# Performance work log

Measured on AMD Instinct MI355X. Metric: run time of the kernel, lower is better.

Reference implementation:

```python
import jax, jax.numpy as jnp
import numpy as np

EPS = 1e-5
SLOPE = 0.01  # LeakyReLU default
C = 512
C2 = C // 2
B, D, W, H = 2, 16, 16, 16


def _leaky(x):
    return jnp.where(x >= 0, x, SLOPE * x)


def _bn_c(x, g, b, rm, rv):
    # per-channel BN (eval mode) over axis 1 of a (B,C,...) tensor
    shape = (1, -1) + (1,) * (x.ndim - 2)
    inv = jax.lax.rsqrt(rv + EPS)
    return (x - rm.reshape(shape)) * (inv * g).reshape(shape) + b.reshape(shape)


def _bn_s(x, g, b, rm, rv):
    # scalar-feature BatchNorm1d(1) in eval mode
    return (x - rm[0]) * (jax.lax.rsqrt(rv[0] + EPS) * g[0]) + b[0]


def setup_inputs() -> dict:
    key = jax.random.key(0)
    ks = jax.random.split(key, 8)
    s = 0.02
    inp = {
        'x': jax.random.normal(ks[0], (B, C, D, W, H), jnp.float32),
        'topo_prompt': jax.random.normal(ks[1], (D, W, H, 6), jnp.float32) * s,
        # edge_aggregation_func: Linear(6,1)+BN1d(1)
        'w_ea': jax.random.normal(ks[2], (1, 6), jnp.float32) * s,
        'b_ea': jnp.zeros((1,), jnp.float32),
        'g_ea': jnp.ones((1,), jnp.float32), 'be_ea': jnp.zeros((1,), jnp.float32),
        'rm_ea': jnp.zeros((1,), jnp.float32), 'rv_ea': jnp.ones((1,), jnp.float32),
        # vertex_update_func: Linear(2C, C/2)+BN1d(C/2)
        'w_v': jax.random.normal(ks[3], (C2, 2 * C), jnp.float32) * s,
        'b_v': jnp.zeros((C2,), jnp.float32),
        'g_v': jnp.ones((C2,), jnp.float32), 'be_v': jnp.zeros((C2,), jnp.float32),
        'rm_v': jnp.zeros((C2,), jnp.float32), 'rv_v': jnp.ones((C2,), jnp.float32),
        # edge_update_func: Linear(2C, C/2)+BN1d(C/2)
        'w_e': jax.random.normal(ks[4], (C2, 2 * C), jnp.float32) * s,
        'b_e': jnp.zeros((C2,), jnp.float32),
        'g_e': jnp.ones((C2,), jnp.float32), 'be_e': jnp.zeros((C2,), jnp.float32),
        'rm_e': jnp.zeros((C2,), jnp.float32), 'rv_e': jnp.ones((C2,), jnp.float32),
        # update_edge_reduce_func: Linear(6,1)+BN1d(1)
        'w_r': jax.random.normal(ks[5], (1, 6), jnp.float32) * s,
        'b_r': jnp.zeros((1,), jnp.float32),
        'g_r': jnp.ones((1,), jnp.float32), 'be_r': jnp.zeros((1,), jnp.float32),
        'rm_r': jnp.zeros((1,), jnp.float32), 'rv_r': jnp.ones((1,), jnp.float32),
        # final_aggregation_layer: Conv3d(3C/2 -> C, k=1, bias=False)+BN3d(C)
        'w_f': jax.random.normal(ks[6], (C, C + C2), jnp.float32) * s,
        'g_f': jnp.ones((C,), jnp.float32), 'be_f': jnp.zeros((C,), jnp.float32),
        'rm_f': jnp.zeros((C,), jnp.float32), 'rv_f': jnp.ones((C,), jnp.float32),
    }
    return inp


def reference(x, topo_prompt,
              w_ea, b_ea, g_ea, be_ea, rm_ea, rv_ea,
              w_v, b_v, g_v, be_v, rm_v, rv_v,
              w_e, b_e, g_e, be_e, rm_e, rv_e,
              w_r, b_r, g_r, be_r, rm_r, rv_r,
              w_f, g_f, be_f, rm_f, rv_f):
    # 6-neighbor circular shifts: cat((x[-1:], x[:-1])) == roll(+1); cat((x[1:], x[:1])) == roll(-1)
    shifts = jnp.stack([
        jnp.roll(x, 1, axis=2), jnp.roll(x, -1, axis=2),
        jnp.roll(x, 1, axis=3), jnp.roll(x, -1, axis=3),
        jnp.roll(x, 1, axis=4), jnp.roll(x, -1, axis=4),
    ], axis=-1)  # (B,C,D,W,H,6)
    edge = shifts * x[..., None] + topo_prompt  # topo_prompt (D,W,H,6) broadcasts

    # edge aggregation: Linear(6->1) + BN1d(1) + LeakyReLU
    agg = jnp.einsum('bcdwhk,k->bcdwh', edge, w_ea[0]) + b_ea[0]
    agg = _leaky(_bn_s(agg, g_ea, be_ea, rm_ea, rv_ea))  # (B,C,D,W,H)

    # vertex update: Linear(2C->C/2) + BN + LeakyReLU
    feat_v = jnp.concatenate([x, agg], axis=1)  # (B,2C,D,W,H)
    uv = jnp.einsum('bcdwh,oc->bodwh', feat_v, w_v) + b_v[None, :, None, None, None]
    uv = _leaky(_bn_c(uv, g_v, be_v, rm_v, rv_v))  # (B,C/2,D,W,H)

    # edge update: cat(vertex x6, edge) on channel dim -> Linear(2C->C/2) + BN + LeakyReLU
    vrep = jnp.broadcast_to(x[..., None], x.shape + (6,))
    feat_e = jnp.concatenate([vrep, edge], axis=1)  # (B,2C,D,W,H,6)
    ue = jnp.einsum('bcdwhk,oc->bodwhk', feat_e, w_e) + b_e[None, :, None, None, None, None]
    ue = _leaky(_bn_c(ue, g_e, be_e, rm_e, rv_e))  # (B,C/2,D,W,H,6)

    # reduce 6 neighbors: Linear(6->1) + BN1d(1) + LeakyReLU
    ur = jnp.einsum('bodwhk,k->bodwh', ue, w_r[0]) + b_r[0]
    ur = _leaky(_bn_s(ur, g_r, be_r, rm_r, rv_r))  # (B,C/2,D,W,H)

    update_feature = uv * ur

    # final 1x1x1 conv (bias=False) + BN3d + LeakyReLU
    fused = jnp.concatenate([x, update_feature], axis=1)  # (B,3C/2,D,W,H)
    out = jnp.einsum('bcdwh,oc->bodwh', fused, w_f)
    out = _leaky(_bn_c(out, g_f, be_f, rm_f, rv_f))
    return out
```

## Files before the change

### kernel.cpp

```cpp
#include <hip/hip_runtime.h>

#define BATCH 2
#define C 512
#define C2 256
#define V 4096
#define NROWS 8192
#define EPS 1e-5f
#define SLOPE 0.01f
#define LDSW 40

typedef __bf16 bf16;
typedef __bf16 bf16x8 __attribute__((ext_vector_type(8)));
typedef __bf16 bf16x4 __attribute__((ext_vector_type(4)));
typedef float  f32x4  __attribute__((ext_vector_type(4)));

__device__ __forceinline__ float leaky(float x) { return x >= 0.f ? x : SLOPE * x; }

__device__ __forceinline__ int nbr(int v, int k) {
    int h = v & 15, w = (v >> 4) & 15, d = v >> 8;
    switch (k) {
        case 0: return (v & 0x0FF) | (((d + 15) & 15) << 8);
        case 1: return (v & 0x0FF) | (((d + 1) & 15) << 8);
        case 2: return (v & 0xF0F) | (((w + 15) & 15) << 4);
        case 3: return (v & 0xF0F) | (((w + 1) & 15) << 4);
        case 4: return (v & 0xFF0) | ((h + 15) & 15);
        default: return (v & 0xFF0) | ((h + 1) & 15);
    }
}

__device__ __forceinline__ void st_lds(bf16* lds, uint4 v, int t) {
    *(uint4*)(lds + (t >> 2) * LDSW + (t & 3) * 8) = v;
}

__device__ __forceinline__ void mm32(const bf16* A, const bf16* B,
                                     f32x4 (&acc)[4][2], int abase, int bbase,
                                     int lr, int kg)
{
    bf16x8 af[4], bv[2];
    #pragma unroll
    for (int mb = 0; mb < 4; mb++)
        af[mb] = *(const bf16x8*)(A + (abase + mb * 16 + lr) * LDSW + kg * 8);
    #pragma unroll
    for (int nb = 0; nb < 2; nb++)
        bv[nb] = *(const bf16x8*)(B + (bbase + nb * 16 + lr) * LDSW + kg * 8);
    #pragma unroll
    for (int mb = 0; mb < 4; mb++)
        #pragma unroll
        for (int nb = 0; nb < 2; nb++)
            acc[mb][nb] = __builtin_amdgcn_mfma_f32_16x16x32_bf16(af[mb], bv[nb], acc[mb][nb], 0, 0, 0);
}

__global__ __launch_bounds__(256) void k_prep(
    const float* wv, const float* we, const float* wf,
    const float* w_ea, const float* b_ea, const float* g_ea, const float* be_ea,
    const float* rm_ea, const float* rv_ea,
    const float* b_v, const float* g_v, const float* be_v, const float* rm_v, const float* rv_v,
    const float* b_e, const float* g_e, const float* be_e, const float* rm_e, const float* rv_e,
    const float* w_r, const float* b_r, const float* g_r, const float* be_r,
    const float* rm_r, const float* rv_r,
    const float* g_f, const float* be_f, const float* rm_f, const float* rv_f,
    float* P, float* obv, float* obe, float* obf,
    bf16* wmain, bf16* we2, bf16* owf)
{
    int i = blockIdx.x * 256 + threadIdx.x;
    if (i < 524288) {
        int o = i >> 10, c = i & 1023;
        float val;
        if (o < 256) val = rsqrtf(rv_v[o] + EPS) * g_v[o] * wv[(size_t)o * 1024 + c];
        else {
            int oe = o - 256;
            val = (c < 512) ? rsqrtf(rv_e[oe] + EPS) * g_e[oe] * we[(size_t)oe * 1024 + c] : 0.f;
        }
        wmain[i] = (bf16)val;
    } else if (i < 655360) {
        int j = i - 524288; int o = j >> 9, c = j & 511;
        we2[j] = (bf16)(rsqrtf(rv_e[o] + EPS) * g_e[o] * we[(size_t)o * 1024 + 512 + c]);
    } else if (i < 1048576) {
        int j = i - 655360; int o = j / 768;
        owf[j] = (bf16)(rsqrtf(rv_f[o] + EPS) * g_f[o] * wf[j]);
    }
    if (blockIdx.x == 0) {
        int t = threadIdx.x;
        obf[t]       = be_f[t]       - rsqrtf(rv_f[t]       + EPS) * g_f[t]       * rm_f[t];
        obf[t + 256] = be_f[t + 256] - rsqrtf(rv_f[t + 256] + EPS) * g_f[t + 256] * rm_f[t + 256];
        float sv = rsqrtf(rv_v[t] + EPS) * g_v[t];
        obv[t] = sv * (b_v[t] - rm_v[t]) + be_v[t];
        float se = rsqrtf(rv_e[t] + EPS) * g_e[t];
        obe[t] = se * (b_e[t] - rm_e[t]) + be_e[t];
        if (t < 6) {
            float sa = rsqrtf(rv_ea[0] + EPS) * g_ea[0];
            P[t] = sa * w_ea[t];
            float sr = rsqrtf(rv_r[0] + EPS) * g_r[0];
            P[8 + t] = sr * w_r[t];
        }
        if (t == 6) {
            float sa = rsqrtf(rv_ea[0] + EPS) * g_ea[0];
            P[6] = sa * (b_ea[0] - rm_ea[0]) + be_ea[0];
            float sr = rsqrtf(rv_r[0] + EPS) * g_r[0];
            P[14] = sr * (b_r[0] - rm_r[0]) + be_r[0];
        }
    }
}

__global__ __launch_bounds__(256) void k_aggT(
    const float* __restrict__ x, const float* __restrict__ topo,
    const float* __restrict__ P,
    bf16* __restrict__ xT, bf16* __restrict__ aggT)
{
    __shared__ float T[64][65];
    const int t = threadIdx.x;
    const int b = blockIdx.z, ct = blockIdx.y * 64, vt = blockIdx.x * 64;
    const int cl = t >> 2;
    const int c  = ct + cl;
    const int vl0 = (t & 3) * 16;
    const int v0 = vt + vl0;
    const int w = (v0 >> 4) & 15, d = v0 >> 8;
    const float* xp = x + (((size_t)b * C + c) << 12);

    float xr[16], xd0[16], xd1[16], xw0[16], xw1[16];
    #pragma unroll
    for (int i = 0; i < 4; i++) {
        float4 a;
        a = ((const float4*)(xp + v0))[i];                        xr [4*i]=a.x; xr [4*i+1]=a.y; xr [4*i+2]=a.z; xr [4*i+3]=a.w;
        a = ((const float4*)(xp + (((d+15)&15)<<8) + (w<<4)))[i]; xd0[4*i]=a.x; xd0[4*i+1]=a.y; xd0[4*i+2]=a.z; xd0[4*i+3]=a.w;
        a = ((const float4*)(xp + (((d+ 1)&15)<<8) + (w<<4)))[i]; xd1[4*i]=a.x; xd1[4*i+1]=a.y; xd1[4*i+2]=a.z; xd1[4*i+3]=a.w;
        a = ((const float4*)(xp + (d<<8) + (((w+15)&15)<<4)))[i]; xw0[4*i]=a.x; xw0[4*i+1]=a.y; xw0[4*i+2]=a.z; xw0[4*i+3]=a.w;
        a = ((const float4*)(xp + (d<<8) + (((w+ 1)&15)<<4)))[i]; xw1[4*i]=a.x; xw1[4*i+1]=a.y; xw1[4*i+2]=a.z; xw1[4*i+3]=a.w;
    }

    #pragma unroll
    for (int p = 0; p < 2; ++p) {
        float val[16];
        if (p == 0) {
            #pragma unroll
            for (int j = 0; j < 16; j++) val[j] = xr[j];
        } else {
            #pragma unroll
            for (int j = 0; j < 16; j++) {
                const float* tp = topo + (size_t)(v0 + j) * 6;
                float s = P[6];
                s = fmaf(P[0], fmaf(xd0[j], xr[j], tp[0]), s);
                s = fmaf(P[1], fmaf(xd1[j], xr[j], tp[1]), s);
                s = fmaf(P[2], fmaf(xw0[j], xr[j], tp[2]), s);
                s = fmaf(P[3], fmaf(xw1[j], xr[j], tp[3]), s);
                s = fmaf(P[4], fmaf(xr[(j+15)&15], xr[j], tp[4]), s);
                s = fmaf(P[5], fmaf(xr[(j+ 1)&15], xr[j], tp[5]), s);
                val[j] = leaky(s);
            }
        }
        __syncthreads();
        #pragma unroll
        for (int j = 0; j < 16; j++) T[cl][vl0 + j] = val[j];
        __syncthreads();
        const int vr = t >> 2, c0 = (t & 3) * 16;
        bf16x8 lo, hi;
        #pragma unroll
        for (int i = 0; i < 8; i++) {
            lo[i] = (bf16)T[c0 + i][vr];
            hi[i] = (bf16)T[c0 + 8 + i][vr];
        }
        bf16* dst = (p == 0) ? xT : aggT;
        bf16* dp = dst + ((size_t)(b << 12) + vt + vr) * C + ct + c0;
        *(bf16x8*)dp = lo;
        *(bf16x8*)(dp + 8) = hi;
    }
}

__global__ __launch_bounds__(512, 4) void k_main(
    const bf16* __restrict__ xT, const bf16* __restrict__ aggT,
    const bf16* __restrict__ wm, const float* __restrict__ bvp,
    bf16* __restrict__ uvT, float* __restrict__ sxe)
{
    __shared__ __align__(16) bf16 L[2][2][128 * LDSW];
    const int t = threadIdx.x, lane = t & 63, wid = t >> 6;
    const int wmi = wid >> 2, wni = wid & 3;
    const int lr = lane & 15, kg = lane >> 4;
    const int n0 = blockIdx.x * 128, m0 = blockIdx.y * 128;
    const int srow = t >> 2, scol = (t & 3) * 8;

    f32x4 acc[4][2];
    #pragma unroll
    for (int mb = 0; mb < 4; mb++)
        #pragma unroll
        for (int nb = 0; nb < 2; nb++) acc[mb][nb] = 0.f;

    uint4 sA, sB;
    auto issue = [&](int s) {
        sA = *(const uint4*)(wm + (size_t)(m0 + srow) * 1024 + s * 32 + scol);
        const bf16* bs = (s < 16) ? xT : aggT;
        sB = *(const uint4*)(bs + (size_t)(n0 + srow) * C + (s & 15) * 32 + scol);
    };

    issue(0);
    st_lds(L[0][0], sA, t); st_lds(L[0][1], sB, t);
    issue(1);
    __syncthreads();
    #pragma unroll 1
    for (int s = 0; s < 32; ++s) {
        mm32(L[s & 1][0], L[s & 1][1], acc, wmi * 64, wni * 32, lr, kg);
        if (s + 1 < 32) {
            st_lds(L[(s + 1) & 1][0], sA, t); st_lds(L[(s + 1) & 1][1], sB, t);
            if (s + 2 < 32) issue(s + 2);
            __syncthreads();
        }
    }

    if (m0 < 256) {
        f32x4 bvv[4];
        #pragma unroll
        for (int mb = 0; mb < 4; mb++)
            bvv[mb] = *(const f32x4*)(bvp + m0 + wmi * 64 + mb * 16 + kg * 4);
        #pragma unroll
        for (int mb = 0; mb < 4; mb++)
            #pragma unroll
            for (int nb = 0; nb < 2; nb++) {
                const int col = n0 + wni * 32 + nb * 16 + lr;
                const int o = m0 + wmi * 64 + mb * 16 + kg * 4;
                bf16x4 o4;
                #pragma unroll
                for (int q = 0; q < 4; q++)
                    o4[q] = (bf16)leaky(acc[mb][nb][q] + bvv[mb][q]);
                *(bf16x4*)(uvT + (size_t)col * C2 + o) = o4;
            }
    } else {
        #pragma unroll
        for (int mb = 0; mb < 4; mb++)
            #pragma unroll
            for (int nb = 0; nb < 2; nb++) {
                const int col = n0 + wni * 32 + nb * 16 + lr;
                const int o = (m0 - 256) + wmi * 64 + mb * 16 + kg * 4;
                *(f32x4*)(sxe + (size_t)col * C2 + o) = acc[mb][nb];
            }
    }
}

__global__ __launch_bounds__(512, 4) void k_edge(
    const bf16* __restrict__ xT, const bf16* __restrict__ we2,
    const float* __restrict__ topo, bf16* __restrict__ se)
{
    __shared__ __align__(16) bf16 L[2][2][128 * LDSW];
    const int t = threadIdx.x, lane = t & 63, wid = t >> 6;
    const int wmi = wid >> 2, wni = wid & 3;
    const int lr = lane & 15, kg = lane >> 4;
    const int n0 = blockIdx.x * 128, m0 = blockIdx.y * 128;
    const int kk = n0 >> 13;
    const int srow = t >> 2, scol = (t & 3) * 8;
    const int r = (n0 & 8191) + srow;
    const int bb = r >> 12, vv = r & 4095;
    const int rn = (bb << 12) | nbr(vv, kk);
    const float tp = topo[vv * 6 + kk];

    f32x4 acc[4][2];
    #pragma unroll
    for (int mb = 0; mb < 4; mb++)
        #pragma unroll
        for (int nb = 0; nb < 2; nb++) acc[mb][nb] = 0.f;

    uint4 sA, sB, sBn;
    auto issue = [&](int s) {
        sA  = *(const uint4*)(we2 + (size_t)(m0 + srow) * 512 + s * 32 + scol);
        sB  = *(const uint4*)(xT + (size_t)r  * C + s * 32 + scol);
        sBn = *(const uint4*)(xT + (size_t)rn * C + s * 32 + scol);
    };
    auto commitB = [&](bf16* lds) {
        bf16x8 xa = *(const bf16x8*)&sB;
        bf16x8 xn = *(const bf16x8*)&sBn;
        bf16x8 e;
        #pragma unroll
        for (int i = 0; i < 8; i++)
            e[i] = (bf16)fmaf((float)xa[i], (float)xn[i], tp);
        *(bf16x8*)(lds + (t >> 2) * LDSW + (t & 3) * 8) = e;
    };

    issue(0);
    st_lds(L[0][0], sA, t); commitB(L[0][1]);
    issue(1);
    __syncthreads();
    #pragma unroll 1
    for (int s = 0; s < 16; ++s) {
        mm32(L[s & 1][0], L[s & 1][1], acc, wmi * 64, wni * 32, lr, kg);
        if (s + 1 < 16) {
            st_lds(L[(s + 1) & 1][0], sA, t); commitB(L[(s + 1) & 1][1]);
            if (s + 2 < 16) issue(s + 2);
            __syncthreads();
        }
    }

    #pragma unroll
    for (int mb = 0; mb < 4; mb++)
        #pragma unroll
        for (int nb = 0; nb < 2; nb++) {
            const int col = n0 + wni * 32 + nb * 16 + lr;
            const int rout = col & 8191;
            const int o = m0 + wmi * 64 + mb * 16 + kg * 4;
            bf16x4 o4;
            #pragma unroll
            for (int q = 0; q < 4; q++) o4[q] = (bf16)acc[mb][nb][q];
            *(bf16x4*)(se + ((size_t)kk * NROWS + rout) * C2 + o) = o4;
        }
}

__global__ __launch_bounds__(256) void k_comb(
    const float* __restrict__ sxe, const bf16* __restrict__ se,
    const bf16* __restrict__ uvT, const float* __restrict__ bep,
    const float* __restrict__ P, bf16* __restrict__ updT)
{
    const int g = blockIdx.x * 256 + threadIdx.x;
    const int row = g >> 5, o0 = (g & 31) * 8;
    const size_t base = (size_t)row * C2 + o0;

    f32x4 sx0 = *(const f32x4*)(sxe + base);
    f32x4 sx1 = *(const f32x4*)(sxe + base + 4);
    f32x4 be0 = *(const f32x4*)(bep + o0);
    f32x4 be1 = *(const f32x4*)(bep + o0 + 4);
    float ur[8] = {};
    #pragma unroll
    for (int k = 0; k < 6; k++) {
        bf16x8 s8 = *(const bf16x8*)(se + (size_t)k * NROWS * C2 + base);
        const float wrk = P[8 + k];
        #pragma unroll
        for (int i = 0; i < 4; i++) {
            ur[i]     = fmaf(wrk, leaky(sx0[i] + (float)s8[i]     + be0[i]), ur[i]);
            ur[i + 4] = fmaf(wrk, leaky(sx1[i] + (float)s8[i + 4] + be1[i]), ur[i + 4]);
        }
    }
    const float brp = P[14];
    bf16x8 uv8 = *(const bf16x8*)(uvT + base);
    bf16x8 o8;
    #pragma unroll
    for (int i = 0; i < 8; i++)
        o8[i] = (bf16)((float)uv8[i] * leaky(ur[i] + brp));
    *(bf16x8*)(updT + base) = o8;
}

__global__ __launch_bounds__(512, 4) void k_out(
    const bf16* __restrict__ xT, const bf16* __restrict__ updT,
    const bf16* __restrict__ wf, const float* __restrict__ bfp,
    float* __restrict__ out)
{
    __shared__ __align__(16) bf16 L[2][2][128 * LDSW];
    const int t = threadIdx.x, lane = t & 63, wid = t >> 6;
    const int wmi = wid >> 2, wni = wid & 3;
    const int lr = lane & 15, kg = lane >> 4;
    const int n0 = blockIdx.x * 128, m0 = blockIdx.y * 128;
    const int srow = t >> 2, scol = (t & 3) * 8;

    f32x4 acc[4][2];
    #pragma unroll
    for (int mb = 0; mb < 4; mb++)
        #pragma unroll
        for (int nb = 0; nb < 2; nb++) acc[mb][nb] = 0.f;

    uint4 sA, sB;
    auto issue = [&](int s) {
        sA = *(const uint4*)(wf + (size_t)(m0 + srow) * 768 + s * 32 + scol);
        if (s < 16) sB = *(const uint4*)(xT   + (size_t)(n0 + srow) * C  + s * 32 + scol);
        else        sB = *(const uint4*)(updT + (size_t)(n0 + srow) * C2 + (s - 16) * 32 + scol);
    };

    issue(0);
    st_lds(L[0][0], sA, t); st_lds(L[0][1], sB, t);
    issue(1);
    __syncthreads();
    #pragma unroll 1
    for (int s = 0; s < 24; ++s) {
        mm32(L[s & 1][0], L[s & 1][1], acc, wmi * 64, wni * 32, lr, kg);
        if (s + 1 < 24) {
            st_lds(L[(s + 1) & 1][0], sA, t); st_lds(L[(s + 1) & 1][1], sB, t);
            if (s + 2 < 24) issue(s + 2);
            __syncthreads();
        }
    }

    f32x4 bfv[4];
    #pragma unroll
    for (int mb = 0; mb < 4; mb++)
        bfv[mb] = *(const f32x4*)(bfp + m0 + wmi * 64 + mb * 16 + kg * 4);
    #pragma unroll
    for (int mb = 0; mb < 4; mb++)
        #pragma unroll
        for (int nb = 0; nb < 2; nb++) {
            const int col = n0 + wni * 32 + nb * 16 + lr;
            const int b = col >> 12, v = col & 4095;
            const int o = m0 + wmi * 64 + mb * 16 + kg * 4;
            #pragma unroll
            for (int q = 0; q < 4; q++)
                out[(((size_t)b * C + o + q) << 12) + v] = leaky(acc[mb][nb][q] + bfv[mb][q]);
        }
}

extern "C" void kernel_launch(void* const* d_in, const int* in_sizes, int n_in,
                              void* d_out, int out_size, void* d_ws, size_t ws_size,
                              hipStream_t stream)
{
    const float* x    = (const float*)d_in[0];
    const float* topo = (const float*)d_in[1];
    const float* w_ea = (const float*)d_in[2];
    const float* b_ea = (const float*)d_in[3];
    const float* g_ea = (const float*)d_in[4];
    const float* be_ea= (const float*)d_in[5];
    const float* rm_ea= (const float*)d_in[6];
    const float* rv_ea= (const float*)d_in[7];
    const float* w_v  = (const float*)d_in[8];
    const float* b_v  = (const float*)d_in[9];
    const float* g_v  = (const float*)d_in[10];
    const float* be_v = (const float*)d_in[11];
    const float* rm_v = (const float*)d_in[12];
    const float* rv_v = (const float*)d_in[13];
    const float* w_e  = (const float*)d_in[14];
    const float* b_e  = (const float*)d_in[15];
    const float* g_e  = (const float*)d_in[16];
    const float* be_e = (const float*)d_in[17];
    const float* rm_e = (const float*)d_in[18];
    const float* rv_e = (const float*)d_in[19];
    const float* w_r  = (const float*)d_in[20];
    const float* b_r  = (const float*)d_in[21];
    const float* g_r  = (const float*)d_in[22];
    const float* be_r = (const float*)d_in[23];
    const float* rm_r = (const float*)d_in[24];
    const float* rv_r = (const float*)d_in[25];
    const float* w_f  = (const float*)d_in[26];
    const float* g_f  = (const float*)d_in[27];
    const float* be_f = (const float*)d_in[28];
    const float* rm_f = (const float*)d_in[29];
    const float* rv_f = (const float*)d_in[30];

    char* base = (char*)d_ws;
    size_t off = 0;
    auto take = [&](size_t bytes) { size_t r = off; off = (off + bytes + 255) & ~(size_t)255; return r; };
    float* P    = (float*)(base + take(64 * 4));
    float* bvp  = (float*)(base + take(256 * 4));
    float* bep  = (float*)(base + take(256 * 4));
    float* bfp  = (float*)(base + take(512 * 4));
    bf16*  wmp  = (bf16*)(base + take((size_t)524288 * 2));
    bf16*  we2p = (bf16*)(base + take((size_t)131072 * 2));
    bf16*  wfp  = (bf16*)(base + take((size_t)393216 * 2));
    bf16*  xT   = (bf16*)(base + take((size_t)NROWS * C * 2));
    bf16*  aggT = (bf16*)(base + take((size_t)NROWS * C * 2));
    bf16*  uvT  = (bf16*)(base + take((size_t)NROWS * C2 * 2));
    bf16*  updT = (bf16*)(base + take((size_t)NROWS * C2 * 2));
    float* sxe  = (float*)(base + take((size_t)NROWS * C2 * 4));
    bf16*  se   = (bf16*)(base + take((size_t)6 * NROWS * C2 * 2));

    k_prep<<<4096, 256, 0, stream>>>(
        w_v, w_e, w_f,
        w_ea, b_ea, g_ea, be_ea, rm_ea, rv_ea,
        b_v, g_v, be_v, rm_v, rv_v,
        b_e, g_e, be_e, rm_e, rv_e,
        w_r, b_r, g_r, be_r, rm_r, rv_r,
        g_f, be_f, rm_f, rv_f,
        P, bvp, bep, bfp, wmp, we2p, wfp);

    k_aggT<<<dim3(64, 8, 2), 256, 0, stream>>>(x, topo, P, xT, aggT);

    k_main<<<dim3(64, 4), 512, 0, stream>>>(xT, aggT, wmp, bvp, uvT, sxe);
    k_edge<<<dim3(384, 2), 512, 0, stream>>>(xT, we2p, topo, se);
    k_comb<<<dim3(NROWS * C2 / 8 / 256), 256, 0, stream>>>(sxe, se, uvT, bep, P, updT);
    k_out<<<dim3(64, 4), 512, 0, stream>>>(xT, updT, wfp, bfp, (float*)d_out);
}
```

Before: 101.4 us.

## Merge vertex and edge GEMMs into one launch with register-direct B operands

Replaces the separate k_main and k_edge launches with a single k_gemm1 grid. Blocks are split by index between the vertex/x-projection GEMM and the six-neighbor edge GEMM. The B operand is no longer staged in LDS: each wave loads its activation fragments straight from global memory into registers in MFMA layout, and only the weight tile goes through double-buffered LDS. It also trims the k-loop for the sxe half to 16 steps and moves to 256-thread blocks with a 4x4 MFMA tile per wave. This should cut launch overhead, LDS traffic and the tail imbalance between the two kernels, at the cost of more VGPRs and uncoalesced 16-byte global loads for B.

```diff
diff --git a/kernel.cpp b/kernel.cpp
--- a/kernel.cpp
+++ b/kernel.cpp
@@ -166,138 +166,156 @@
     }
 }
 
-__global__ __launch_bounds__(512, 4) void k_main(
+template<bool MAIN>
+__device__ __forceinline__ void gemm_body(
+    int m0, int n0, int kk, int nsteps,
+    const bf16* __restrict__ wA, int ldA,
     const bf16* __restrict__ xT, const bf16* __restrict__ aggT,
-    const bf16* __restrict__ wm, const float* __restrict__ bvp,
-    bf16* __restrict__ uvT, float* __restrict__ sxe)
-{
-    __shared__ __align__(16) bf16 L[2][2][128 * LDSW];
-    const int t = threadIdx.x, lane = t & 63, wid = t >> 6;
-    const int wmi = wid >> 2, wni = wid & 3;
+    const float* __restrict__ topo, const float* __restrict__ bvp,
+    bf16* __restrict__ uvT, float* __restrict__ sxe, bf16* __restrict__ se,
+    bf16 (*A)[128 * LDSW])
+{
+    const int t = threadIdx.x, lane = t & 63;
+    const int wv = t >> 6, wmi = wv >> 1, wni = wv & 1;
     const int lr = lane & 15, kg = lane >> 4;
-    const int n0 = blockIdx.x * 128, m0 = blockIdx.y * 128;
-    const int srow = t >> 2, scol = (t & 3) * 8;
-
-    f32x4 acc[4][2];
-    #pragma unroll
-    for (int mb = 0; mb < 4; mb++)
-        #pragma unroll
-        for (int nb = 0; nb < 2; nb++) acc[mb][nb] = 0.f;
-
-    uint4 sA, sB;
-    auto issue = [&](int s) {
-        sA = *(const uint4*)(wm + (size_t)(m0 + srow) * 1024 + s * 32 + scol);
-        const bf16* bs = (s < 16) ? xT : aggT;
-        sB = *(const uint4*)(bs + (size_t)(n0 + srow) * C + (s & 15) * 32 + scol);
-    };
-
-    issue(0);
-    st_lds(L[0][0], sA, t); st_lds(L[0][1], sB, t);
-    issue(1);
+
+    const bf16* pB[4]; const bf16* pB2[4]; float tp[4]; int colv[4];
+    #pragma unroll
+    for (int nb = 0; nb < 4; nb++) {
+        int row = n0 + wni * 64 + nb * 16 + lr;
+        colv[nb] = row;
+        pB[nb] = xT + (size_t)row * C + kg * 8;
+        if (MAIN) {
+            pB2[nb] = aggT + (size_t)row * C + kg * 8;
+        } else {
+            int v = row & 4095, bb = row >> 12;
+            pB2[nb] = xT + (size_t)((bb << 12) | nbr(v, kk)) * C + kg * 8;
+            tp[nb] = topo[v * 6 + kk];
+        }
+    }
+
+    f32x4 acc[4][4];
+    #pragma unroll
+    for (int mb = 0; mb < 4; mb++)
+        #pragma unroll
+        for (int nb = 0; nb < 4; nb++) acc[mb][nb] = 0.f;
+
+    const int arow = t >> 1, acol = (t & 1) * 16;
+    const bf16* pA = wA + (size_t)(m0 + arow) * ldA + acol;
+
+    uint4 a0 = *(const uint4*)(pA);
+    uint4 a1 = *(const uint4*)(pA + 8);
+    uint4 bA[4], bN[4];
+    #pragma unroll
+    for (int nb = 0; nb < 4; nb++) {
+        bA[nb] = *(const uint4*)(pB[nb]);
+        if (!MAIN) bN[nb] = *(const uint4*)(pB2[nb]);
+    }
+    *(uint4*)(&A[0][arow * LDSW + acol])     = a0;
+    *(uint4*)(&A[0][arow * LDSW + acol + 8]) = a1;
     __syncthreads();
+
     #pragma unroll 1
-    for (int s = 0; s < 32; ++s) {
-        mm32(L[s & 1][0], L[s & 1][1], acc, wmi * 64, wni * 32, lr, kg);
-        if (s + 1 < 32) {
-            st_lds(L[(s + 1) & 1][0], sA, t); st_lds(L[(s + 1) & 1][1], sB, t);
-            if (s + 2 < 32) issue(s + 2);
-            __syncthreads();
-        }
-    }
-
-    if (m0 < 256) {
-        f32x4 bvv[4];
+    for (int s = 0; s < nsteps; ++s) {
+        bf16x8 Bc[4];
+        #pragma unroll
+        for (int nb = 0; nb < 4; nb++) {
+            if (MAIN) {
+                Bc[nb] = *(bf16x8*)&bA[nb];
+            } else {
+                bf16x8 xa = *(bf16x8*)&bA[nb], xn = *(bf16x8*)&bN[nb];
+                #pragma unroll
+                for (int i = 0; i < 8; i++)
+                    Bc[nb][i] = (bf16)fmaf((float)xa[i], (float)xn[i], tp[nb]);
+            }
+        }
+        if (s + 1 < nsteps) {
+            const int sc = s + 1;
+            a0 = *(const uint4*)(pA + sc * 32);
+            a1 = *(const uint4*)(pA + sc * 32 + 8);
+            const int off = (sc & 15) * 32;
+            #pragma unroll
+            for (int nb = 0; nb < 4; nb++) {
+                const bf16* src = (MAIN && sc >= 16) ? pB2[nb] : pB[nb];
+                bA[nb] = *(const uint4*)(src + off);
+                if (!MAIN) bN[nb] = *(const uint4*)(pB2[nb] + off);
+            }
+        }
+        bf16x8 af[4];
         #pragma unroll
         for (int mb = 0; mb < 4; mb++)
-            bvv[mb] = *(const f32x4*)(bvp + m0 + wmi * 64 + mb * 16 + kg * 4);
+            af[mb] = *(const bf16x8*)(&A[s & 1][(wmi * 64 + mb * 16 + lr) * LDSW + kg * 8]);
         #pragma unroll
         for (int mb = 0; mb < 4; mb++)
             #pragma unroll
-            for (int nb = 0; nb < 2; nb++) {
-                const int col = n0 + wni * 32 + nb * 16 + lr;
+            for (int nb = 0; nb < 4; nb++)
+                acc[mb][nb] = __builtin_amdgcn_mfma_f32_16x16x32_bf16(af[mb], Bc[nb], acc[mb][nb], 0, 0, 0);
+        if (s + 1 < nsteps) {
+            *(uint4*)(&A[(s + 1) & 1][arow * LDSW + acol])     = a0;
+            *(uint4*)(&A[(s + 1) & 1][arow * LDSW + acol + 8]) = a1;
+        }
+        __syncthreads();
+    }
+
+    if (MAIN) {
+        if (m0 < 256) {
+            #pragma unroll
+            for (int mb = 0; mb < 4; mb++) {
                 const int o = m0 + wmi * 64 + mb * 16 + kg * 4;
+                f32x4 bv4 = *(const f32x4*)(bvp + o);
+                #pragma unroll
+                for (int nb = 0; nb < 4; nb++) {
+                    bf16x4 o4;
+                    #pragma unroll
+                    for (int q = 0; q < 4; q++)
+                        o4[q] = (bf16)leaky(acc[mb][nb][q] + bv4[q]);
+                    *(bf16x4*)(uvT + (size_t)colv[nb] * C2 + o) = o4;
+                }
+            }
+        } else {
+            #pragma unroll
+            for (int mb = 0; mb < 4; mb++) {
+                const int o = (m0 - 256) + wmi * 64 + mb * 16 + kg * 4;
+                #pragma unroll
+                for (int nb = 0; nb < 4; nb++)
+                    *(f32x4*)(sxe + (size_t)colv[nb] * C2 + o) = acc[mb][nb];
+            }
+        }
+    } else {
+        #pragma unroll
+        for (int mb = 0; mb < 4; mb++) {
+            const int o = m0 + wmi * 64 + mb * 16 + kg * 4;
+            #pragma unroll
+            for (int nb = 0; nb < 4; nb++) {
                 bf16x4 o4;
                 #pragma unroll
-                for (int q = 0; q < 4; q++)
-                    o4[q] = (bf16)leaky(acc[mb][nb][q] + bvv[mb][q]);
-                *(bf16x4*)(uvT + (size_t)col * C2 + o) = o4;
-            }
+                for (int q = 0; q < 4; q++) o4[q] = (bf16)acc[mb][nb][q];
+                *(bf16x4*)(se + ((size_t)kk * NROWS + colv[nb]) * C2 + o) = o4;
+            }
+        }
+    }
+}
+
+__global__ __launch_bounds__(256, 3) void k_gemm1(
+    const bf16* __restrict__ xT, const bf16* __restrict__ aggT,
+    const bf16* __restrict__ wm, const bf16* __restrict__ we2,
+    const float* __restrict__ bvp, const float* __restrict__ topo,
+    bf16* __restrict__ uvT, float* __restrict__ sxe, bf16* __restrict__ se)
+{
+    __shared__ __align__(16) bf16 A[2][128 * LDSW];
+    const int bid = blockIdx.x;
+    if (bid < 256) {
+        const int m0 = (bid >> 6) * 128, n0 = (bid & 63) * 128;
+        const int nsteps = (m0 < 256) ? 32 : 16;
+        gemm_body<true>(m0, n0, 0, nsteps, wm, 1024, xT, aggT, topo, bvp,
+                        uvT, sxe, nullptr, A);
     } else {
-        #pragma unroll
-        for (int mb = 0; mb < 4; mb++)
-            #pragma unroll
-            for (int nb = 0; nb < 2; nb++) {
-                const int col = n0 + wni * 32 + nb * 16 + lr;
-                const int o = (m0 - 256) + wmi * 64 + mb * 16 + kg * 4;
-                *(f32x4*)(sxe + (size_t)col * C2 + o) = acc[mb][nb];
-            }
-    }
-}
-
-__global__ __launch_bounds__(512, 4) void k_edge(
-    const bf16* __restrict__ xT, const bf16* __restrict__ we2,
-    const float* __restrict__ topo, bf16* __restrict__ se)
-{
-    __shared__ __align__(16) bf16 L[2][2][128 * LDSW];
-    const int t = threadIdx.x, lane = t & 63, wid = t >> 6;
-    const int wmi = wid >> 2, wni = wid & 3;
-    const int lr = lane & 15, kg = lane >> 4;
-    const int n0 = blockIdx.x * 128, m0 = blockIdx.y * 128;
-    const int kk = n0 >> 13;
-    const int srow = t >> 2, scol = (t & 3) * 8;
-    const int r = (n0 & 8191) + srow;
-    const int bb = r >> 12, vv = r & 4095;
-    const int rn = (bb << 12) | nbr(vv, kk);
-    const float tp = topo[vv * 6 + kk];
-
-    f32x4 acc[4][2];
-    #pragma unroll
-    for (int mb = 0; mb < 4; mb++)
-        #pragma unroll
-        for (int nb = 0; nb < 2; nb++) acc[mb][nb] = 0.f;
-
-    uint4 sA, sB, sBn;
-    auto issue = [&](int s) {
-        sA  = *(const uint4*)(we2 + (size_t)(m0 + srow) * 512 + s * 32 + scol);
-        sB  = *(const uint4*)(xT + (size_t)r  * C + s * 32 + scol);
-        sBn = *(const uint4*)(xT + (size_t)rn * C + s * 32 + scol);
-    };
-    auto commitB = [&](bf16* lds) {
-        bf16x8 xa = *(const bf16x8*)&sB;
-        bf16x8 xn = *(const bf16x8*)&sBn;
-        bf16x8 e;
-        #pragma unroll
-        for (int i = 0; i < 8; i++)
-            e[i] = (bf16)fmaf((float)xa[i], (float)xn[i], tp);
-        *(bf16x8*)(lds + (t >> 2) * LDSW + (t & 3) * 8) = e;
-    };
-
-    issue(0);
-    st_lds(L[0][0], sA, t); commitB(L[0][1]);
-    issue(1);
-    __syncthreads();
-    #pragma unroll 1
-    for (int s = 0; s < 16; ++s) {
-        mm32(L[s & 1][0], L[s & 1][1], acc, wmi * 64, wni * 32, lr, kg);
-        if (s + 1 < 16) {
-            st_lds(L[(s + 1) & 1][0], sA, t); commitB(L[(s + 1) & 1][1]);
-            if (s + 2 < 16) issue(s + 2);
-            __syncthreads();
-        }
-    }
-
-    #pragma unroll
-    for (int mb = 0; mb < 4; mb++)
-        #pragma unroll
-        for (int nb = 0; nb < 2; nb++) {
-            const int col = n0 + wni * 32 + nb * 16 + lr;
-            const int rout = col & 8191;
-            const int o = m0 + wmi * 64 + mb * 16 + kg * 4;
-            bf16x4 o4;
-            #pragma unroll
-            for (int q = 0; q < 4; q++) o4[q] = (bf16)acc[mb][nb][q];
-            *(bf16x4*)(se + ((size_t)kk * NROWS + rout) * C2 + o) = o4;
-        }
+        const int e = bid - 256;
+        const int m0 = (e / 384) * 128;
+        const int r = e % 384, kk = r >> 6, n0 = (r & 63) * 128;
+        gemm_body<false>(m0, n0, kk, 16, we2, 512, xT, aggT, topo, bvp,
+                         nullptr, nullptr, se, A);
+    }
 }
 
 __global__ __launch_bounds__(256) void k_comb(
@@ -453,8 +471,7 @@
 
     k_aggT<<<dim3(64, 8, 2), 256, 0, stream>>>(x, topo, P, xT, aggT);
 
-    k_main<<<dim3(64, 4), 512, 0, stream>>>(xT, aggT, wmp, bvp, uvT, sxe);
-    k_edge<<<dim3(384, 2), 512, 0, stream>>>(xT, we2p, topo, se);
+    k_gemm1<<<dim3(1024), 256, 0, stream>>>(xT, aggT, wmp, we2p, bvp, topo, uvT, sxe, se);
     k_comb<<<dim3(NROWS * C2 / 8 / 256), 256, 0, stream>>>(sxe, se, uvT, bep, P, updT);
     k_out<<<dim3(64, 4), 512, 0, stream>>>(xT, updT, wfp, bfp, (float*)d_out);
 }
```

New measurement: 144.3 us. +42.3%, slower.
